# Kernel tuning notes

Measured on AMD Instinct MI355X. Metric: run time of the kernel, lower is better.

## Reference

```python
import jax, jax.numpy as jnp
import numpy as np

N_NODES = 100000
N_EDGES = 1600000
IN_CH = 128
OUT_CH = 128


def setup_inputs() -> dict:
    key = jax.random.key(0)
    k1, k2, k3, k4, k5, k6 = jax.random.split(key, 6)
    x = jax.random.normal(k1, (N_NODES, IN_CH), dtype=jnp.float32)
    weight = jax.random.normal(k2, (IN_CH, OUT_CH), dtype=jnp.float32) * (1.0 / np.sqrt(IN_CH))
    bias = jax.random.uniform(k3, (OUT_CH,), dtype=jnp.float32)
    edge_row = jax.random.randint(k4, (N_EDGES,), 0, N_NODES, dtype=jnp.int64)
    edge_col = jax.random.randint(k5, (N_EDGES,), 0, N_NODES, dtype=jnp.int64)
    edge_weight = jax.random.uniform(k6, (N_EDGES,), dtype=jnp.float32)
    return {"x": x, "weight": weight, "bias": bias,
            "edge_row": edge_row, "edge_col": edge_col, "edge_weight": edge_weight}


def reference(x, weight, bias, edge_row, edge_col, edge_weight):
    # Dense transform: [N, in] @ [in, out] -> [N, out]
    h = x @ weight
    # SpMM: out[r] = sum_e w_e * h[c_e] for edges (r, c) -- gather + scatter-add
    msgs = edge_weight[:, None] * h[edge_col]          # [E, out]
    agg = jax.ops.segment_sum(msgs, edge_row, num_segments=N_NODES)  # [N, out]
    return agg + bias
```

## Files before the change

### kernel.cpp

```cpp
#include <hip/hip_runtime.h>

#define N_NODES 100000
#define N_EDGES_MAX 1600000
#define IN_CH 128
#define OUT_CH 128
#define NB 391
#define BLK_E 2048
#define NBLK_MAX ((N_EDGES_MAX + BLK_E - 1) / BLK_E)
#define NBLK_P 800
#define CAP_LDS 5120

constexpr size_t align_up(size_t x) { return (x + 255) & ~size_t(255); }
constexpr size_t H_OFF     = 0;
constexpr size_t H_SZ      = (size_t)N_NODES * OUT_CH * 2;
constexpr size_t BREC_OFF  = align_up(H_OFF + H_SZ);
constexpr size_t BREC_SZ   = (size_t)N_EDGES_MAX * 8;
constexpr size_t SREC_OFF  = align_up(BREC_OFF + BREC_SZ);
constexpr size_t BLK_OFF   = align_up(SREC_OFF + BREC_SZ);
constexpr size_t BLK_SZ    = (size_t)NB * NBLK_P * 4;
constexpr size_t BTOT_OFF  = align_up(BLK_OFF + BLK_SZ);
constexpr size_t BTOT_SZ   = (size_t)NB * 4;
constexpr size_t BBASE_OFF = align_up(BTOT_OFF + BTOT_SZ);
constexpr size_t BBASE_SZ  = (size_t)(NB + 1) * 4;
constexpr size_t RS_OFF    = align_up(BBASE_OFF + BBASE_SZ);
constexpr size_t RS_SZ     = (size_t)(N_NODES + 1) * 4;
constexpr size_t WS_NEED   = RS_OFF + RS_SZ;

__device__ __forceinline__ unsigned short f2bf(float f) {
    unsigned u = __float_as_uint(f);
    return (unsigned short)((u + 0x7FFFu + ((u >> 16) & 1u)) >> 16);
}
__device__ __forceinline__ float bf2f(unsigned short b) {
    return __uint_as_float((unsigned)b << 16);
}
__device__ __forceinline__ float bflo(unsigned u) { return __uint_as_float(u << 16); }
__device__ __forceinline__ float bfhi(unsigned u) { return __uint_as_float(u & 0xFFFF0000u); }

__device__ __forceinline__ void accum8(float4& a0, float4& a1, const uint4 hv,
                                       const float wt) {
    a0.x += wt * bflo(hv.x); a0.y += wt * bfhi(hv.x);
    a0.z += wt * bflo(hv.y); a0.w += wt * bfhi(hv.y);
    a1.x += wt * bflo(hv.z); a1.y += wt * bfhi(hv.z);
    a1.z += wt * bflo(hv.w); a1.w += wt * bfhi(hv.w);
}

__global__ __launch_bounds__(256) void gemm_xw(const float* __restrict__ x,
                                               const float* __restrict__ W,
                                               unsigned short* __restrict__ h) {
    __shared__ float Wl[128 * 128];
    __shared__ float Xl[32 * 128];
    const int t = threadIdx.x;

    const float4* W4 = (const float4*)W;
    float4* Wl4 = (float4*)Wl;
#pragma unroll
    for (int i = 0; i < 16; ++i) Wl4[t + 256 * i] = W4[t + 256 * i];

    const long rbase = (long)blockIdx.x * 32;
    const float4* x4 = (const float4*)(x + rbase * IN_CH);
    float4* Xl4 = (float4*)Xl;
#pragma unroll
    for (int i = 0; i < 4; ++i) Xl4[t + 256 * i] = x4[t + 256 * i];

    __syncthreads();

    const int tx = t & 31;
    const int ty = t >> 5;
    float acc[4][4];
#pragma unroll
    for (int i = 0; i < 4; ++i)
#pragma unroll
        for (int j = 0; j < 4; ++j) acc[i][j] = 0.f;

    for (int k = 0; k < 128; ++k) {
        float4 w = *(const float4*)&Wl[k * 128 + tx * 4];
        float xv[4];
#pragma unroll
        for (int i = 0; i < 4; ++i) xv[i] = Xl[(ty * 4 + i) * 128 + k];
#pragma unroll
        for (int i = 0; i < 4; ++i) {
            acc[i][0] += xv[i] * w.x;
            acc[i][1] += xv[i] * w.y;
            acc[i][2] += xv[i] * w.z;
            acc[i][3] += xv[i] * w.w;
        }
    }

#pragma unroll
    for (int i = 0; i < 4; ++i) {
        long r = rbase + ty * 4 + i;
        ushort4 o;
        o.x = f2bf(acc[i][0]); o.y = f2bf(acc[i][1]);
        o.z = f2bf(acc[i][2]); o.w = f2bf(acc[i][3]);
        *(ushort4*)&h[r * OUT_CH + tx * 4] = o;
    }
}

__global__ __launch_bounds__(256) void bucket_hist(const int* __restrict__ erow,
                                                   unsigned* __restrict__ blkcnt,
                                                   int n) {
    __shared__ unsigned cnt[NB];
    const int t = threadIdx.x, p = blockIdx.x;
    for (int i = t; i < NB; i += 256) cnt[i] = 0u;
    __syncthreads();
    const int e0 = p * BLK_E;
#pragma unroll
    for (int j = 0; j < 8; ++j) {
        int e = e0 + j * 256 + t;
        if (e < n) atomicAdd(&cnt[(unsigned)erow[e] >> 8], 1u);
    }
    __syncthreads();
    for (int i = t; i < NB; i += 256) blkcnt[(size_t)i * NBLK_P + p] = cnt[i];
}

__global__ __launch_bounds__(256) void scan_col(unsigned* __restrict__ blkcnt,
                                                unsigned* __restrict__ btotal,
                                                int nblk) {
    __shared__ unsigned part[256];
    const int b = blockIdx.x, t = threadIdx.x;
    unsigned* col = blkcnt + (size_t)b * NBLK_P;
    unsigned v[4];
    unsigned sum = 0;
    const int p0 = t * 4;
#pragma unroll
    for (int j = 0; j < 4; ++j) {
        int p = p0 + j;
        v[j] = (p < nblk) ? col[p] : 0u;
        sum += v[j];
    }
    part[t] = sum;
    __syncthreads();
    for (int off = 1; off < 256; off <<= 1) {
        unsigned a = (t >= off) ? part[t - off] : 0u;
        __syncthreads();
        part[t] += a;
        __syncthreads();
    }
    unsigned excl = part[t] - sum;
#pragma unroll
    for (int j = 0; j < 4; ++j) {
        int p = p0 + j;
        if (p < nblk) { unsigned tv = v[j]; col[p] = excl; excl += tv; }
    }
    if (t == 255) btotal[b] = part[255];
}

__global__ __launch_bounds__(512) void scan_buckets(const unsigned* __restrict__ btotal,
                                                    unsigned* __restrict__ bbase,
                                                    unsigned* __restrict__ row_start,
                                                    int n_edges) {
    __shared__ unsigned s[512];
    const int t = threadIdx.x;
    unsigned v = (t < NB) ? btotal[t] : 0u;
    s[t] = v;
    __syncthreads();
    for (int off = 1; off < 512; off <<= 1) {
        unsigned a = (t >= off) ? s[t - off] : 0u;
        __syncthreads();
        s[t] += a;
        __syncthreads();
    }
    if (t < NB) bbase[t] = s[t] - v;
    if (t == 0) {
        bbase[NB] = (unsigned)n_edges;
        row_start[N_NODES] = (unsigned)n_edges;
    }
}

__global__ __launch_bounds__(256) void bucket_scatter(const int* __restrict__ erow,
                                                      const int* __restrict__ ecol,
                                                      const float* __restrict__ ew,
                                                      const unsigned* __restrict__ blkbase,
                                                      const unsigned* __restrict__ bbase,
                                                      uint2* __restrict__ brec,
                                                      int n) {
    __shared__ unsigned cnt[NB];
    __shared__ unsigned basec[NB];
    const int t = threadIdx.x, p = blockIdx.x;
    for (int i = t; i < NB; i += 256) {
        cnt[i] = 0u;
        basec[i] = bbase[i] + blkbase[(size_t)i * NBLK_P + p];
    }
    __syncthreads();
    const int e0 = p * BLK_E;
#pragma unroll
    for (int j = 0; j < 8; ++j) {
        int e = e0 + j * 256 + t;
        if (e < n) {
            unsigned r = (unsigned)erow[e];
            unsigned c = (unsigned)ecol[e];
            float w = ew[e];
            unsigned bk = r >> 8;
            unsigned rank = atomicAdd(&cnt[bk], 1u);
            brec[basec[bk] + rank] =
                make_uint2(((r & 255u) << 17) | c, __float_as_uint(w));
        }
    }
}

__global__ __launch_bounds__(256) void row_scatter(const uint2* __restrict__ brec,
                                                   const unsigned* __restrict__ bbase,
                                                   unsigned* __restrict__ row_start,
                                                   uint2* __restrict__ srec) {
    __shared__ unsigned hist[256], sc[256], cur[256];
    __shared__ uint2 recs[CAP_LDS];
    const int b = blockIdx.x, t = threadIdx.x;
    const unsigned s = bbase[b], e = bbase[b + 1];
    const unsigned m = e - s;
    hist[t] = 0u;
    __syncthreads();
    const bool fits = (m <= CAP_LDS);
    if (fits) {
        for (unsigned i = t; i < m; i += 256) {
            uint2 rc = brec[s + i];
            recs[i] = rc;
            atomicAdd(&hist[rc.x >> 17], 1u);
        }
    } else {
        for (unsigned i = t; i < m; i += 256)
            atomicAdd(&hist[brec[s + i].x >> 17], 1u);
    }
    __syncthreads();
    unsigned v = hist[t];
    sc[t] = v;
    __syncthreads();
    for (int off = 1; off < 256; off <<= 1) {
        unsigned a = (t >= off) ? sc[t - off] : 0u;
        __syncthreads();
        sc[t] += a;
        __syncthreads();
    }
    const unsigned gpos = s + sc[t] - v;
    const int grow = b * 256 + t;
    if (grow < N_NODES) row_start[grow] = gpos;
    cur[t] = gpos;
    __syncthreads();
    if (fits) {
        for (unsigned i = t; i < m; i += 256) {
            uint2 rc = recs[i];
            unsigned pos = atomicAdd(&cur[rc.x >> 17], 1u);
            srec[pos] = make_uint2(rc.x & 0x1FFFFu, rc.y);
        }
    } else {
        for (unsigned i = t; i < m; i += 256) {
            uint2 rc = brec[s + i];
            unsigned pos = atomicAdd(&cur[rc.x >> 17], 1u);
            srec[pos] = make_uint2(rc.x & 0x1FFFFu, rc.y);
        }
    }
}

__global__ __launch_bounds__(256) void aggregate(const unsigned short* __restrict__ h,
                                                 const uint2* __restrict__ srec,
                                                 const unsigned* __restrict__ row_start,
                                                 const float* __restrict__ bias,
                                                 float* __restrict__ out) {
    const int t = threadIdx.x, lane = t & 15;
    const int r = blockIdx.x * 16 + (t >> 4);
    if (r >= N_NODES) return;
    const unsigned s = row_start[r], e = row_start[r + 1];

    const float4* b4 = (const float4*)bias;
    float4 a0 = b4[lane * 2];
    float4 a1 = b4[lane * 2 + 1];

    const uint4* h16 = (const uint4*)h;

    unsigned i = s;
    for (; i + 4 <= e; i += 4) {
        uint2 r0 = srec[i];
        uint2 r1 = srec[i + 1];
        uint2 r2 = srec[i + 2];
        uint2 r3 = srec[i + 3];
        uint4 v0 = h16[(size_t)r0.x * 16 + lane];
        uint4 v1 = h16[(size_t)r1.x * 16 + lane];
        uint4 v2 = h16[(size_t)r2.x * 16 + lane];
        uint4 v3 = h16[(size_t)r3.x * 16 + lane];
        accum8(a0, a1, v0, __uint_as_float(r0.y));
        accum8(a0, a1, v1, __uint_as_float(r1.y));
        accum8(a0, a1, v2, __uint_as_float(r2.y));
        accum8(a0, a1, v3, __uint_as_float(r3.y));
    }
    for (; i < e; ++i) {
        uint2 rc = srec[i];
        uint4 vv = h16[(size_t)rc.x * 16 + lane];
        accum8(a0, a1, vv, __uint_as_float(rc.y));
    }

    float4* o = (float4*)(out + (size_t)r * OUT_CH + lane * 8);
    o[0] = a0;
    o[1] = a1;
}

__global__ __launch_bounds__(256) void init_bias(float* __restrict__ out,
                                                 const float* __restrict__ bias) {
    int idx = blockIdx.x * 256 + threadIdx.x;
    float4 b = ((const float4*)bias)[idx & 31];
    ((float4*)out)[idx] = b;
}

__global__ __launch_bounds__(256) void spmm_scatter(const unsigned short* __restrict__ h,
                                                    const int* __restrict__ erow,
                                                    const int* __restrict__ ecol,
                                                    const float* __restrict__ ew,
                                                    float* __restrict__ out,
                                                    int n_edges) {
    const int t = threadIdx.x;
    const int lane = t & 31;
    const int e = blockIdx.x * 8 + (t >> 5);
    if (e >= n_edges) return;
    const int r = erow[e];
    const int c = ecol[e];
    const float w = ew[e];
    ushort4 hv = ((const ushort4*)(h + (size_t)c * OUT_CH))[lane];
    float* o = out + (size_t)r * OUT_CH + lane * 4;
    atomicAdd(o + 0, w * bf2f(hv.x));
    atomicAdd(o + 1, w * bf2f(hv.y));
    atomicAdd(o + 2, w * bf2f(hv.z));
    atomicAdd(o + 3, w * bf2f(hv.w));
}

extern "C" void kernel_launch(void* const* d_in, const int* in_sizes, int n_in,
                              void* d_out, int out_size, void* d_ws, size_t ws_size,
                              hipStream_t stream) {
    const float* x    = (const float*)d_in[0];
    const float* W    = (const float*)d_in[1];
    const float* bias = (const float*)d_in[2];
    const int*   erow = (const int*)d_in[3];
    const int*   ecol = (const int*)d_in[4];
    const float* ew   = (const float*)d_in[5];
    float* out = (float*)d_out;
    const int n_edges = in_sizes[3];

    char* ws = (char*)d_ws;
    unsigned short* h  = (unsigned short*)(ws + H_OFF);
    uint2*    brec     = (uint2*)(ws + BREC_OFF);
    uint2*    srec     = (uint2*)(ws + SREC_OFF);
    unsigned* blkcnt   = (unsigned*)(ws + BLK_OFF);
    unsigned* btotal   = (unsigned*)(ws + BTOT_OFF);
    unsigned* bbase    = (unsigned*)(ws + BBASE_OFF);
    unsigned* rowstart = (unsigned*)(ws + RS_OFF);

    gemm_xw<<<N_NODES / 32, 256, 0, stream>>>(x, W, h);

    const int nblk = (n_edges + BLK_E - 1) / BLK_E;
    if (ws_size >= WS_NEED && n_edges <= N_EDGES_MAX) {
        bucket_hist<<<nblk, 256, 0, stream>>>(erow, blkcnt, n_edges);
        scan_col<<<NB, 256, 0, stream>>>(blkcnt, btotal, nblk);
        scan_buckets<<<1, 512, 0, stream>>>(btotal, bbase, rowstart, n_edges);
        bucket_scatter<<<nblk, 256, 0, stream>>>(erow, ecol, ew, blkcnt, bbase,
                                                 brec, n_edges);
        row_scatter<<<NB, 256, 0, stream>>>(brec, bbase, rowstart, srec);
        aggregate<<<(N_NODES + 15) / 16, 256, 0, stream>>>(h, srec, rowstart,
                                                           bias, out);
    } else {
        init_bias<<<(N_NODES * 32) / 256, 256, 0, stream>>>(out, bias);
        spmm_scatter<<<(n_edges + 7) / 8, 256, 0, stream>>>(h, erow, ecol, ew,
                                                            out, n_edges);
    }
}
```

Measured before the change: 164.6 us.

## Replace FP32 SIMT GEMM with bf16 MFMA GEMM using pre-transposed weights

```diff
diff --git a/kernel.cpp b/kernel.cpp
--- a/kernel.cpp
+++ b/kernel.cpp
@@ -6,9 +6,11 @@
 #define OUT_CH 128
 #define NB 391
 #define BLK_E 2048
-#define NBLK_MAX ((N_EDGES_MAX + BLK_E - 1) / BLK_E)
 #define NBLK_P 800
 #define CAP_LDS 5120
+
+typedef __attribute__((ext_vector_type(8))) short bf16x8_t;
+typedef __attribute__((ext_vector_type(4))) float f32x4_t;
 
 constexpr size_t align_up(size_t x) { return (x + 255) & ~size_t(255); }
 constexpr size_t H_OFF     = 0;
@@ -24,7 +26,9 @@
 constexpr size_t BBASE_SZ  = (size_t)(NB + 1) * 4;
 constexpr size_t RS_OFF    = align_up(BBASE_OFF + BBASE_SZ);
 constexpr size_t RS_SZ     = (size_t)(N_NODES + 1) * 4;
-constexpr size_t WS_NEED   = RS_OFF + RS_SZ;
+constexpr size_t WT_OFF    = align_up(RS_OFF + RS_SZ);
+constexpr size_t WT_SZ     = (size_t)IN_CH * OUT_CH * 2;
+constexpr size_t WS_NEED   = WT_OFF + WT_SZ;
 
 __device__ __forceinline__ unsigned short f2bf(float f) {
     unsigned u = __float_as_uint(f);
@@ -44,55 +48,55 @@
     a1.z += wt * bflo(hv.w); a1.w += wt * bfhi(hv.w);
 }
 
-__global__ __launch_bounds__(256) void gemm_xw(const float* __restrict__ x,
-                                               const float* __restrict__ W,
-                                               unsigned short* __restrict__ h) {
-    __shared__ float Wl[128 * 128];
-    __shared__ float Xl[32 * 128];
-    const int t = threadIdx.x;
-
-    const float4* W4 = (const float4*)W;
-    float4* Wl4 = (float4*)Wl;
-#pragma unroll
-    for (int i = 0; i < 16; ++i) Wl4[t + 256 * i] = W4[t + 256 * i];
-
-    const long rbase = (long)blockIdx.x * 32;
-    const float4* x4 = (const float4*)(x + rbase * IN_CH);
-    float4* Xl4 = (float4*)Xl;
-#pragma unroll
-    for (int i = 0; i < 4; ++i) Xl4[t + 256 * i] = x4[t + 256 * i];
-
-    __syncthreads();
-
-    const int tx = t & 31;
-    const int ty = t >> 5;
-    float acc[4][4];
-#pragma unroll
-    for (int i = 0; i < 4; ++i)
-#pragma unroll
-        for (int j = 0; j < 4; ++j) acc[i][j] = 0.f;
-
-    for (int k = 0; k < 128; ++k) {
-        float4 w = *(const float4*)&Wl[k * 128 + tx * 4];
-        float xv[4];
-#pragma unroll
-        for (int i = 0; i < 4; ++i) xv[i] = Xl[(ty * 4 + i) * 128 + k];
-#pragma unroll
-        for (int i = 0; i < 4; ++i) {
-            acc[i][0] += xv[i] * w.x;
-            acc[i][1] += xv[i] * w.y;
-            acc[i][2] += xv[i] * w.z;
-            acc[i][3] += xv[i] * w.w;
-        }
-    }
-
-#pragma unroll
-    for (int i = 0; i < 4; ++i) {
-        long r = rbase + ty * 4 + i;
-        ushort4 o;
-        o.x = f2bf(acc[i][0]); o.y = f2bf(acc[i][1]);
-        o.z = f2bf(acc[i][2]); o.w = f2bf(acc[i][3]);
-        *(ushort4*)&h[r * OUT_CH + tx * 4] = o;
+__global__ __launch_bounds__(256) void prep_wt(const float* __restrict__ W,
+                                               unsigned short* __restrict__ wt) {
+    const int idx = blockIdx.x * 256 + threadIdx.x;
+    const float w = W[idx];
+    const int k = idx >> 7, c = idx & 127;
+    wt[c * 128 + k] = f2bf(w);
+}
+
+__global__ __launch_bounds__(256) void gemm_mfma(const float* __restrict__ x,
+                                                 const unsigned short* __restrict__ wt,
+                                                 unsigned short* __restrict__ h) {
+    const int wv = threadIdx.x >> 6;
+    const int l  = threadIdx.x & 63;
+    const int lr = l & 15;
+    const int lk = (l >> 4) * 8;
+    const long rbase = (long)blockIdx.x * 64 + wv * 16;
+
+    f32x4_t acc[8];
+#pragma unroll
+    for (int i = 0; i < 8; ++i) acc[i] = (f32x4_t){0.f, 0.f, 0.f, 0.f};
+
+    long arow = rbase + lr;
+    if (arow >= N_NODES) arow = N_NODES - 1;
+    const float4* xr = (const float4*)(x + arow * IN_CH);
+
+    for (int kc = 0; kc < 128; kc += 32) {
+        float4 f0 = xr[(kc + lk) >> 2];
+        float4 f1 = xr[((kc + lk) >> 2) + 1];
+        bf16x8_t a;
+        a[0] = (short)f2bf(f0.x); a[1] = (short)f2bf(f0.y);
+        a[2] = (short)f2bf(f0.z); a[3] = (short)f2bf(f0.w);
+        a[4] = (short)f2bf(f1.x); a[5] = (short)f2bf(f1.y);
+        a[6] = (short)f2bf(f1.z); a[7] = (short)f2bf(f1.w);
+#pragma unroll
+        for (int ct = 0; ct < 8; ++ct) {
+            bf16x8_t b = *(const bf16x8_t*)&wt[(size_t)(ct * 16 + lr) * 128 + kc + lk];
+            acc[ct] = __builtin_amdgcn_mfma_f32_16x16x32_bf16(a, b, acc[ct], 0, 0, 0);
+        }
+    }
+
+    const int r0 = (l >> 4) * 4;
+#pragma unroll
+    for (int ct = 0; ct < 8; ++ct) {
+        const int col = ct * 16 + lr;
+#pragma unroll
+        for (int reg = 0; reg < 4; ++reg) {
+            long r = rbase + r0 + reg;
+            if (r < N_NODES) h[r * OUT_CH + col] = f2bf(acc[ct][reg]);
+        }
     }
 }
 
@@ -290,6 +294,52 @@
     float4* o = (float4*)(out + (size_t)r * OUT_CH + lane * 8);
     o[0] = a0;
     o[1] = a1;
+}
+
+__global__ __launch_bounds__(256) void gemm_xw(const float* __restrict__ x,
+                                               const float* __restrict__ W,
+                                               unsigned short* __restrict__ h) {
+    __shared__ float Wl[128 * 128];
+    __shared__ float Xl[32 * 128];
+    const int t = threadIdx.x;
+    const float4* W4 = (const float4*)W;
+    float4* Wl4 = (float4*)Wl;
+#pragma unroll
+    for (int i = 0; i < 16; ++i) Wl4[t + 256 * i] = W4[t + 256 * i];
+    const long rbase = (long)blockIdx.x * 32;
+    const float4* x4 = (const float4*)(x + rbase * IN_CH);
+    float4* Xl4 = (float4*)Xl;
+#pragma unroll
+    for (int i = 0; i < 4; ++i) Xl4[t + 256 * i] = x4[t + 256 * i];
+    __syncthreads();
+    const int tx = t & 31;
+    const int ty = t >> 5;
+    float acc[4][4];
+#pragma unroll
+    for (int i = 0; i < 4; ++i)
+#pragma unroll
+        for (int j = 0; j < 4; ++j) acc[i][j] = 0.f;
+    for (int k = 0; k < 128; ++k) {
+        float4 w = *(const float4*)&Wl[k * 128 + tx * 4];
+        float xv[4];
+#pragma unroll
+        for (int i = 0; i < 4; ++i) xv[i] = Xl[(ty * 4 + i) * 128 + k];
+#pragma unroll
+        for (int i = 0; i < 4; ++i) {
+            acc[i][0] += xv[i] * w.x;
+            acc[i][1] += xv[i] * w.y;
+            acc[i][2] += xv[i] * w.z;
+            acc[i][3] += xv[i] * w.w;
+        }
+    }
+#pragma unroll
+    for (int i = 0; i < 4; ++i) {
+        long r = rbase + ty * 4 + i;
+        ushort4 o;
+        o.x = f2bf(acc[i][0]); o.y = f2bf(acc[i][1]);
+        o.z = f2bf(acc[i][2]); o.w = f2bf(acc[i][3]);
+        *(ushort4*)&h[r * OUT_CH + tx * 4] = o;
+    }
 }
 
 __global__ __launch_bounds__(256) void init_bias(float* __restrict__ out,
@@ -340,11 +390,12 @@
     unsigned* btotal   = (unsigned*)(ws + BTOT_OFF);
     unsigned* bbase    = (unsigned*)(ws + BBASE_OFF);
     unsigned* rowstart = (unsigned*)(ws + RS_OFF);
-
-    gemm_xw<<<N_NODES / 32, 256, 0, stream>>>(x, W, h);
+    unsigned short* wt = (unsigned short*)(ws + WT_OFF);
 
     const int nblk = (n_edges + BLK_E - 1) / BLK_E;
     if (ws_size >= WS_NEED && n_edges <= N_EDGES_MAX) {
+        prep_wt<<<64, 256, 0, stream>>>(W, wt);
+        gemm_mfma<<<(N_NODES + 63) / 64, 256, 0, stream>>>(x, wt, h);
         bucket_hist<<<nblk, 256, 0, stream>>>(erow, blkcnt, n_edges);
         scan_col<<<NB, 256, 0, stream>>>(blkcnt, btotal, nblk);
         scan_buckets<<<1, 512, 0, stream>>>(btotal, bbase, rowstart, n_edges);
@@ -354,6 +405,7 @@
         aggregate<<<(N_NODES + 15) / 16, 256, 0, stream>>>(h, srec, rowstart,
                                                            bias, out);
     } else {
+        gemm_xw<<<N_NODES / 32, 256, 0, stream>>>(x, W, h);
         init_bias<<<(N_NODES * 32) / 256, 256, 0, stream>>>(out, bias);
         spmm_scatter<<<(n_edges + 7) / 8, 256, 0, stream>>>(h, erow, ecol, ew,
                                                             out, n_edges);
```

Result: faster. 155.6 us (-5.4%).
